# Kernel tuning notes

Measured on AMD Instinct MI355X. Metric: run time of the kernel, lower is better.

Reference implementation:

```python
import jax, jax.numpy as jnp
import numpy as np

B, C, L = 32, 128, 4096
LEVEL = 3
FL = 9            # filter_length (odd so lengths are preserved)
DIM = 512
REG = 0.01        # reg_factor
PAD = (FL - 1) // 2


def _conv1d(x, w, b, padding):
    # x:[B,Cin,L], w:[Cout,Cin,K] -> [B,Cout,L'] (torch cross-correlation)
    y = jax.lax.conv_general_dilated(x, w, (1,), [(padding, padding)],
                                     dimension_numbers=('NCH', 'OIH', 'NCH'))
    return y + b[None, :, None]


def _dywan(approx, stat_w, stat_b, wg1_w, wg1_b, wg2_w, wg2_b):
    feat = jnp.mean(approx, axis=2)                                   # AdaptiveAvgPool1d(1) -> [B,C]
    h = jax.nn.gelu(feat @ stat_w.T + stat_b, approximate=False)
    h = jax.nn.gelu(h @ wg1_w.T + wg1_b, approximate=False)
    filt = h @ wg2_w.T + wg2_b                                        # [B, 2*FL]
    lo_f, hi_f = filt[:, :FL], filt[:, FL:]
    # smoothness: conv1d with kernel [-1,1], zero padding 1 -> forward differences of zero-padded lo_f
    lo_pad = jnp.pad(lo_f, ((0, 0), (1, 1)))
    lo_smooth = jnp.mean(jnp.abs(lo_pad[:, 1:] - lo_pad[:, :-1]))     # length FL+1
    # orthogonality constraint
    lo_n = lo_f / (jnp.linalg.norm(lo_f, axis=1, keepdims=True) + 1e-8)
    shift_loss = 0.0
    for s in (1, 2, 3):
        sh = jnp.roll(lo_n, s, axis=1)
        shift_loss = shift_loss + jnp.mean(jnp.abs(lo_n[:, :, None] * sh[:, None, :]))
    amp_loss = jnp.mean(jnp.abs(jnp.sum(lo_n * lo_n, axis=1) - 1.0))
    ortho = REG * (shift_loss + amp_loss) + 0.1 * lo_smooth
    return lo_f, hi_f, ortho


def _persample_depthwise(x, filt):
    # per-sample filter shared across channels; torch grouped conv groups=B*C.
    # out[b,c,t] = sum_k filt[b,k] * x_pad[b,c,t+k]
    xp = jnp.pad(x, ((0, 0), (0, 0), (PAD, PAD)), mode='edge')        # replicate pad
    Lx = x.shape[2]
    out = jnp.zeros_like(x)
    for k in range(FL):
        out = out + filt[:, k, None, None] * xp[:, :, k:k + Lx]
    return out


def _forward(x, stat_w, stat_b, wg1_w, wg1_b, wg2_w, wg2_b,
             gates_w, gates_b, attn1_w, attn1_b, attn2_w, attn2_b):
    filters = []
    details = []
    approx = x
    ortho_loss = 0.0
    for _ in range(LEVEL):
        lo_f, hi_f, ortho_loss = _dywan(approx, stat_w, stat_b, wg1_w, wg1_b, wg2_w, wg2_b)
        filters.append((lo_f, hi_f))
        new_approx = _persample_depthwise(approx, lo_f)
        detail = _persample_depthwise(approx, hi_f)
        details.append(detail)
        approx = new_approx
    # CrossScaleFusion
    current = approx
    enhanced = []
    for i in range(LEVEL - 1, -1, -1):
        detail = details[i]
        if i < LEVEL - 1:  # attention branches exist only for i < levels-1
            a = jax.nn.gelu(_conv1d(current, attn1_w[i], attn1_b[i], 0), approximate=False)
            attn = jax.nn.sigmoid(_conv1d(a, attn2_w[i], attn2_b[i], 0))
            detail = detail * attn + detail
        gate = jax.nn.sigmoid(_conv1d(current, gates_w[i], gates_b[i], 1))
        current = current + gate * detail
        enhanced.append(detail)
    enhanced.reverse()
    combined = jnp.concatenate([current] + enhanced, axis=1)          # [B,(1+LEVEL)*C,L]
    # ODE is a no-op in the original forward: ode_out = combined
    yl = combined[:, :C, :]
    yh = [combined[:, C * (i + 1):C * (i + 2), :] for i in range(LEVEL)]
    # energy loss under no_grad: dx_dt == 0 -> mse(0, -0) == 0 (computed faithfully)
    cg = jax.lax.stop_gradient(combined)
    dx_dt = jnp.zeros_like(cg)
    dE = 2.0 * jnp.mean(cg * dx_dt, axis=(1, 2))
    diss = jnp.mean(dx_dt * dx_dt, axis=(1, 2))
    energy_loss = jnp.mean((dE + diss) ** 2)
    lo_all = jnp.stack([f[0] for f in filters])                       # [LEVEL,B,FL]
    hi_all = jnp.stack([f[1] for f in filters])
    return yl, yh[0], yh[1], yh[2], ortho_loss, energy_loss, lo_all, hi_all


def setup_inputs() -> dict:
    key = jax.random.key(0)
    ks = jax.random.split(key, 16)
    s = 0.05
    return {
        'x': jax.random.normal(ks[0], (B, C, L), jnp.float32),
        'stat_w': jax.random.normal(ks[1], (DIM, C), jnp.float32) * s,
        'stat_b': jnp.zeros((DIM,), jnp.float32),
        'wg1_w': jax.random.normal(ks[2], (2 * DIM, DIM), jnp.float32) * s,
        'wg1_b': jnp.zeros((2 * DIM,), jnp.float32),
        'wg2_w': jax.random.normal(ks[3], (2 * FL, 2 * DIM), jnp.float32) * s,
        'wg2_b': jnp.zeros((2 * FL,), jnp.float32),
        'gates_w': jax.random.normal(ks[4], (LEVEL, C, C, 3), jnp.float32) * s,
        'gates_b': jnp.zeros((LEVEL, C), jnp.float32),
        'attn1_w': jax.random.normal(ks[5], (LEVEL - 1, C // 4, C, 1), jnp.float32) * s,
        'attn1_b': jnp.zeros((LEVEL - 1, C // 4), jnp.float32),
        'attn2_w': jax.random.normal(ks[6], (LEVEL - 1, C, C // 4, 1), jnp.float32) * s,
        'attn2_b': jnp.zeros((LEVEL - 1, C), jnp.float32),
    }


def reference(x, stat_w, stat_b, wg1_w, wg1_b, wg2_w, wg2_b,
              gates_w, gates_b, attn1_w, attn1_b, attn2_w, attn2_b):
    return _forward(x, stat_w, stat_b, wg1_w, wg1_b, wg2_w, wg2_b,
                    gates_w, gates_b, attn1_w, attn1_b, attn2_w, attn2_b)
```

## Files before the change

kernel.cpp:

```cpp
#include <hip/hip_runtime.h>

#define B_   32
#define C_   128
#define L_   4096
#define FL_  9
#define DIM_ 512
#define BCL  ((size_t)B_ * C_ * L_)

typedef __attribute__((ext_vector_type(8))) short short8;
typedef __attribute__((ext_vector_type(4))) float f32x4;

__device__ __forceinline__ float gelu_f(float x) {
    return 0.5f * x * (1.0f + erff(x * 0.70710678118654752440f));
}
__device__ __forceinline__ float sigm_f(float x) {
    return 1.0f / (1.0f + expf(-x));
}
__device__ __forceinline__ unsigned short bf16_rne(float x) {
    unsigned int u = __float_as_uint(x);
    u += 0x7fffu + ((u >> 16) & 1u);
    return (unsigned short)(u >> 16);
}
__device__ __forceinline__ float bf16_to_f(unsigned short h) {
    return __uint_as_float(((unsigned int)h) << 16);
}

__global__ __launch_bounds__(256) void prep_weights(
    const float* __restrict__ gw, const float* __restrict__ a1w, const float* __restrict__ a2w,
    unsigned short* __restrict__ wgh, unsigned short* __restrict__ wgl,
    unsigned short* __restrict__ a1h, unsigned short* __restrict__ a1l,
    unsigned short* __restrict__ a2h, unsigned short* __restrict__ a2l) {
    int i = blockIdx.x * 256 + threadIdx.x;
    float v; unsigned short* ph; unsigned short* pl; int idx;
    if (i < 147456) {
        int lev = i / 49152, r = i % 49152;
        int co = r / 384, k = r % 384, kp = k >> 7, ci = k & 127;
        v = gw[(((size_t)lev * C_ + co) * C_ + ci) * 3 + kp];
        ph = wgh; pl = wgl; idx = i;
    } else if (i < 147456 + 8192) {
        idx = i - 147456;
        v = a1w[idx];
        ph = a1h; pl = a1l;
    } else if (i < 147456 + 16384) {
        idx = i - 147456 - 8192;
        v = a2w[idx];
        ph = a2h; pl = a2l;
    } else return;
    unsigned short h = bf16_rne(v);
    unsigned short l = bf16_rne(v - bf16_to_f(h));
    ph[idx] = h; pl[idx] = l;
}

__device__ __forceinline__ float block_sum_256(float v, float* red) {
    #pragma unroll
    for (int off = 32; off > 0; off >>= 1) v += __shfl_down(v, off);
    const int wv = threadIdx.x >> 6, ln = threadIdx.x & 63;
    if (ln == 0) red[wv] = v;
    __syncthreads();
    return red[0] + red[1] + red[2] + red[3];
}

__global__ __launch_bounds__(256) void mean_kernel(const float* __restrict__ in,
                                                   float* __restrict__ feat_sum) {
    __shared__ float red[4];
    const int bc = blockIdx.x, t = threadIdx.x;
    const float4* p = (const float4*)(in + (size_t)bc * L_);
    float v = 0.f;
    #pragma unroll
    for (int it = 0; it < L_ / 1024; it++) {
        float4 x = p[t + 256 * it];
        v += x.x + x.y + x.z + x.w;
    }
    float tot = block_sum_256(v, red);
    if (t == 0) feat_sum[bc] = tot;
}

template <int K, int ACT>
__global__ __launch_bounds__(256) void mlp_layer(
    const float* __restrict__ X, const float* __restrict__ W,
    const float* __restrict__ bias, float* __restrict__ Y,
    int N, float xscale) {
    constexpr int PL = K / 64;
    const int w = threadIdx.x >> 6, ln = threadIdx.x & 63;
    const int s = blockIdx.y;
    const int o0 = blockIdx.x * 16 + w * 4;
    float xv[PL];
    const float* xr = X + (size_t)s * K + ln * PL;
    if constexpr (PL == 2) {
        float2 v = *(const float2*)xr;
        xv[0] = v.x * xscale; xv[1] = v.y * xscale;
    } else {
        #pragma unroll
        for (int i = 0; i < PL / 4; i++) {
            float4 v = *(const float4*)(xr + 4 * i);
            xv[4*i] = v.x * xscale; xv[4*i+1] = v.y * xscale;
            xv[4*i+2] = v.z * xscale; xv[4*i+3] = v.w * xscale;
        }
    }
    #pragma unroll
    for (int r = 0; r < 4; r++) {
        int o = o0 + r;
        if (o < N) {
            const float* wr = W + (size_t)o * K + ln * PL;
            float acc = 0.f;
            if constexpr (PL == 2) {
                float2 v = *(const float2*)wr;
                acc = v.x * xv[0] + v.y * xv[1];
            } else {
                #pragma unroll
                for (int i = 0; i < PL / 4; i++) {
                    float4 v = *(const float4*)(wr + 4 * i);
                    acc += v.x * xv[4*i] + v.y * xv[4*i+1] + v.z * xv[4*i+2] + v.w * xv[4*i+3];
                }
            }
            #pragma unroll
            for (int off = 32; off > 0; off >>= 1) acc += __shfl_xor(acc, off);
            if (ln == 0) {
                acc += bias[o];
                Y[(size_t)s * N + o] = ACT ? gelu_f(acc) : acc;
            }
        }
    }
}

__global__ __launch_bounds__(256) void mlp_l3(
    const float* __restrict__ X, const float* __restrict__ W, const float* __restrict__ bias,
    float* __restrict__ lo_out, float* __restrict__ hi_out) {
    constexpr int K = 2 * DIM_, PL = K / 64;
    const int w = threadIdx.x >> 6, ln = threadIdx.x & 63;
    const int s = blockIdx.y;
    const int o0 = blockIdx.x * 16 + w * 4;
    float xv[PL];
    const float* xr = X + (size_t)s * K + ln * PL;
    #pragma unroll
    for (int i = 0; i < PL / 4; i++) {
        float4 v = *(const float4*)(xr + 4 * i);
        xv[4*i] = v.x; xv[4*i+1] = v.y; xv[4*i+2] = v.z; xv[4*i+3] = v.w;
    }
    #pragma unroll
    for (int r = 0; r < 4; r++) {
        int o = o0 + r;
        if (o < 2 * FL_) {
            const float* wr = W + (size_t)o * K + ln * PL;
            float acc = 0.f;
            #pragma unroll
            for (int i = 0; i < PL / 4; i++) {
                float4 v = *(const float4*)(wr + 4 * i);
                acc += v.x * xv[4*i] + v.y * xv[4*i+1] + v.z * xv[4*i+2] + v.w * xv[4*i+3];
            }
            #pragma unroll
            for (int off = 32; off > 0; off >>= 1) acc += __shfl_xor(acc, off);
            if (ln == 0) {
                acc += bias[o];
                if (o < FL_) lo_out[s * FL_ + o] = acc;
                else         hi_out[s * FL_ + (o - FL_)] = acc;
            }
        }
    }
}

__global__ __launch_bounds__(256) void dwconv_kernel(
    const float* __restrict__ in, const float* __restrict__ lo_f, const float* __restrict__ hi_f,
    float* __restrict__ out_lo, float* __restrict__ out_hi, float* __restrict__ feat_next) {
    __shared__ float s[1032];
    __shared__ float red[4];
    const int t = threadIdx.x;
    const int l0 = blockIdx.x * 1024;
    const int c = blockIdx.y, b = blockIdx.z;
    const size_t base = ((size_t)b * C_ + c) * L_;
    *(float4*)&s[4 + 4 * t] = *(const float4*)&in[base + l0 + 4 * t];
    if (t < 4) {
        int gl = l0 - 4 + t;
        s[t] = in[base + max(gl, 0)];
    } else if (t < 8) {
        int i = t - 4;
        s[1028 + i] = in[base + min(l0 + 1024 + i, L_ - 1)];
    }
    float lo[FL_], hi[FL_];
    #pragma unroll
    for (int k = 0; k < FL_; k++) { lo[k] = lo_f[b * FL_ + k]; hi[k] = hi_f[b * FL_ + k]; }
    __syncthreads();
    float oL[4] = {0, 0, 0, 0}, oH[4] = {0, 0, 0, 0};
    #pragma unroll
    for (int k = 0; k < FL_; k++) {
        #pragma unroll
        for (int r = 0; r < 4; r++) {
            float v = s[4 * t + r + k];
            oL[r] += lo[k] * v; oH[r] += hi[k] * v;
        }
    }
    *(float4*)&out_lo[base + l0 + 4 * t] = *(float4*)oL;
    *(float4*)&out_hi[base + l0 + 4 * t] = *(float4*)oH;
    if (feat_next) {
        float tot = block_sum_256(oL[0] + oL[1] + oL[2] + oL[3], red);
        if (t == 0) atomicAdd(&feat_next[b * C_ + c], tot);
    }
}

__global__ void ortho_kernel(const float* __restrict__ lo2, float* __restrict__ scal) {
    const int t = threadIdx.x;
    float smooth = 0.f, sabs2 = 0.f, amp = 0.f;
    if (t < B_) {
        const float* lo = lo2 + t * FL_;
        float ss = 0.f, sa = 0.f, sm = 0.f, prev = 0.f;
        #pragma unroll
        for (int k = 0; k < FL_; k++) {
            float v = lo[k];
            sm += fabsf(v - prev); prev = v;
            ss += v * v; sa += fabsf(v);
        }
        sm += fabsf(prev);
        float den = sqrtf(ss) + 1e-8f;
        float san = sa / den;
        sabs2 = san * san;
        amp = fabsf(ss / (den * den) - 1.0f);
        smooth = sm;
    }
    #pragma unroll
    for (int off = 32; off > 0; off >>= 1) {
        smooth += __shfl_down(smooth, off);
        sabs2  += __shfl_down(sabs2, off);
        amp    += __shfl_down(amp, off);
    }
    if (t == 0) {
        float lo_smooth = smooth / (float)(B_ * 10);
        float shift = 3.0f * (sabs2 / (float)B_) / 81.0f;
        scal[0] = 0.01f * (shift + amp / (float)B_) + 0.1f * lo_smooth;
        scal[1] = 0.0f;
    }
}

#define LT   64
#define SX   136
#define SA   40
template <bool HAS_ATTN>
__global__ __launch_bounds__(256, 2) void recon_kernel(
    const float* __restrict__ cur_in, const float* __restrict__ det_in,
    float* __restrict__ det_out, float* __restrict__ cur_out,
    const unsigned short* __restrict__ wgh, const unsigned short* __restrict__ wgl,
    const float* __restrict__ gb,
    const unsigned short* __restrict__ a1h, const unsigned short* __restrict__ a1l,
    const float* __restrict__ b1,
    const unsigned short* __restrict__ a2h, const unsigned short* __restrict__ a2l,
    const float* __restrict__ b2) {
    __shared__ __attribute__((aligned(16))) unsigned short Xh[(LT + 2) * SX];
    __shared__ __attribute__((aligned(16))) unsigned short Xl[(LT + 2) * SX];
    __shared__ __attribute__((aligned(16))) unsigned short aTh[LT * SA];
    __shared__ __attribute__((aligned(16))) unsigned short aTl[LT * SA];

    const int t = threadIdx.x;
    const int b = blockIdx.y;
    const int l0 = blockIdx.x * LT;
    const float* curb = cur_in + (size_t)b * (C_ * L_);

    for (int u = t; u < 64 * (LT + 2); u += 256) {
        int cp = u / (LT + 2), li = u - cp * (LT + 2);
        int gl = l0 - 1 + li;
        float v0 = 0.f, v1 = 0.f;
        if (gl >= 0 && gl < L_) {
            v0 = curb[(size_t)(2 * cp) * L_ + gl];
            v1 = curb[(size_t)(2 * cp + 1) * L_ + gl];
        }
        unsigned short h0 = bf16_rne(v0), h1 = bf16_rne(v1);
        unsigned short e0 = bf16_rne(v0 - bf16_to_f(h0)), e1 = bf16_rne(v1 - bf16_to_f(h1));
        ((unsigned int*)Xh)[li * (SX / 2) + cp] = (unsigned int)h0 | ((unsigned int)h1 << 16);
        ((unsigned int*)Xl)[li * (SX / 2) + cp] = (unsigned int)e0 | ((unsigned int)e1 << 16);
    }
    __syncthreads();

    const int w = t >> 6, ln = t & 15, q = (t >> 4) & 3;

    f32x4 acc[2][4];
    #pragma unroll
    for (int tm = 0; tm < 2; tm++)
        #pragma unroll
        for (int tn = 0; tn < 4; tn++) acc[tm][tn] = (f32x4){0.f, 0.f, 0.f, 0.f};

    #pragma unroll 2
    for (int kk = 0; kk < 12; kk++) {
        const int kp = kk >> 2, ci0 = (kk & 3) * 32;
        short8 ah[2], al[2];
        #pragma unroll
        for (int tm = 0; tm < 2; tm++) {
            int row = 32 * w + 16 * tm + ln;
            ah[tm] = *(const short8*)&wgh[row * 384 + kk * 32 + q * 8];
            al[tm] = *(const short8*)&wgl[row * 384 + kk * 32 + q * 8];
        }
        #pragma unroll
        for (int tn = 0; tn < 4; tn++) {
            int lrow = 16 * tn + ln + kp;
            const short8 bh = *(const short8*)&Xh[lrow * SX + ci0 + q * 8];
            const short8 bl = *(const short8*)&Xl[lrow * SX + ci0 + q * 8];
            #pragma unroll
            for (int tm = 0; tm < 2; tm++) {
                acc[tm][tn] = __builtin_amdgcn_mfma_f32_16x16x32_bf16(ah[tm], bh, acc[tm][tn], 0, 0, 0);
                acc[tm][tn] = __builtin_amdgcn_mfma_f32_16x16x32_bf16(ah[tm], bl, acc[tm][tn], 0, 0, 0);
                acc[tm][tn] = __builtin_amdgcn_mfma_f32_16x16x32_bf16(al[tm], bh, acc[tm][tn], 0, 0, 0);
            }
        }
    }

    f32x4 dpv[2][4];
    #pragma unroll
    for (int tm = 0; tm < 2; tm++)
        #pragma unroll
        for (int tn = 0; tn < 4; tn++) {
            #pragma unroll
            for (int r = 0; r < 4; r++) {
                int co = 32 * w + 16 * tm + 4 * q + r;
                dpv[tm][tn][r] = det_in[((size_t)b * C_ + co) * L_ + l0 + 16 * tn + ln];
            }
        }

    if (HAS_ATTN) {
        f32x4 acc1[2];
        acc1[0] = (f32x4){0.f, 0.f, 0.f, 0.f};
        acc1[1] = (f32x4){0.f, 0.f, 0.f, 0.f};
        #pragma unroll
        for (int kc = 0; kc < 4; kc++) {
            int ci0 = kc * 32;
            int lrow = 16 * w + ln + 1;
            const short8 bh = *(const short8*)&Xh[lrow * SX + ci0 + q * 8];
            const short8 bl = *(const short8*)&Xl[lrow * SX + ci0 + q * 8];
            #pragma unroll
            for (int tm = 0; tm < 2; tm++) {
                int row = 16 * tm + ln;
                short8 fh = *(const short8*)&a1h[row * 128 + ci0 + q * 8];
                short8 fl = *(const short8*)&a1l[row * 128 + ci0 + q * 8];
                acc1[tm] = __builtin_amdgcn_mfma_f32_16x16x32_bf16(fh, bh, acc1[tm], 0, 0, 0);
                acc1[tm] = __builtin_amdgcn_mfma_f32_16x16x32_bf16(fh, bl, acc1[tm], 0, 0, 0);
                acc1[tm] = __builtin_amdgcn_mfma_f32_16x16x32_bf16(fl, bh, acc1[tm], 0, 0, 0);
            }
        }
        #pragma unroll
        for (int tm = 0; tm < 2; tm++) {
            #pragma unroll
            for (int r = 0; r < 4; r++) {
                int c32 = 16 * tm + 4 * q + r;
                int lcol = 16 * w + ln;
                float v = gelu_f(acc1[tm][r] + b1[c32]);
                unsigned short h = bf16_rne(v);
                aTh[lcol * SA + c32] = h;
                aTl[lcol * SA + c32] = bf16_rne(v - bf16_to_f(h));
            }
        }
        __syncthreads();
        f32x4 acc2[2][4];
        short8 fh2[2], fl2[2];
        #pragma unroll
        for (int tm = 0; tm < 2; tm++) {
            int row = 32 * w + 16 * tm + ln;
            fh2[tm] = *(const short8*)&a2h[row * 32 + q * 8];
            fl2[tm] = *(const short8*)&a2l[row * 32 + q * 8];
            #pragma unroll
            for (int tn = 0; tn < 4; tn++) acc2[tm][tn] = (f32x4){0.f, 0.f, 0.f, 0.f};
        }
        #pragma unroll
        for (int tn = 0; tn < 4; tn++) {
            int lrow = 16 * tn + ln;
            const short8 bh = *(const short8*)&aTh[lrow * SA + q * 8];
            const short8 bl = *(const short8*)&aTl[lrow * SA + q * 8];
            #pragma unroll
            for (int tm = 0; tm < 2; tm++) {
                acc2[tm][tn] = __builtin_amdgcn_mfma_f32_16x16x32_bf16(fh2[tm], bh, acc2[tm][tn], 0, 0, 0);
                acc2[tm][tn] = __builtin_amdgcn_mfma_f32_16x16x32_bf16(fh2[tm], bl, acc2[tm][tn], 0, 0, 0);
                acc2[tm][tn] = __builtin_amdgcn_mfma_f32_16x16x32_bf16(fl2[tm], bh, acc2[tm][tn], 0, 0, 0);
            }
        }
        #pragma unroll
        for (int tm = 0; tm < 2; tm++)
            #pragma unroll
            for (int tn = 0; tn < 4; tn++) {
                #pragma unroll
                for (int r = 0; r < 4; r++) {
                    int co = 32 * w + 16 * tm + 4 * q + r;
                    float at = sigm_f(acc2[tm][tn][r] + b2[co]);
                    float d = dpv[tm][tn][r];
                    d = d * at + d;
                    dpv[tm][tn][r] = d;
                    det_out[((size_t)b * C_ + co) * L_ + l0 + 16 * tn + ln] = d;
                }
            }
    }

    #pragma unroll
    for (int tm = 0; tm < 2; tm++)
        #pragma unroll
        for (int tn = 0; tn < 4; tn++) {
            #pragma unroll
            for (int r = 0; r < 4; r++) {
                int co = 32 * w + 16 * tm + 4 * q + r;
                int lrow = 16 * tn + ln + 1;
                float cur = bf16_to_f(Xh[lrow * SX + co]) + bf16_to_f(Xl[lrow * SX + co]);
                float g = sigm_f(acc[tm][tn][r] + gb[co]);
                cur_out[((size_t)b * C_ + co) * L_ + l0 + 16 * tn + ln] = cur + g * dpv[tm][tn][r];
            }
        }
}

static inline void run_mlp(const float* feat, const float* stat_w, const float* stat_b,
                           const float* wg1_w, const float* wg1_b,
                           const float* wg2_w, const float* wg2_b,
                           float* h1_g, float* h2_g, float* lo_out, float* hi_out,
                           hipStream_t stream) {
    mlp_layer<C_, 1><<<dim3(DIM_ / 16, B_), 256, 0, stream>>>(
        feat, stat_w, stat_b, h1_g, DIM_, 1.0f / (float)L_);
    mlp_layer<DIM_, 1><<<dim3(2 * DIM_ / 16, B_), 256, 0, stream>>>(
        h1_g, wg1_w, wg1_b, h2_g, 2 * DIM_, 1.0f);
    mlp_l3<<<dim3(2, B_), 256, 0, stream>>>(h2_g, wg2_w, wg2_b, lo_out, hi_out);
}

extern "C" void kernel_launch(void* const* d_in, const int* in_sizes, int n_in,
                              void* d_out, int out_size, void* d_ws, size_t ws_size,
                              hipStream_t stream) {
    (void)in_sizes; (void)n_in; (void)out_size; (void)ws_size;
    const float* x       = (const float*)d_in[0];
    const float* stat_w  = (const float*)d_in[1];
    const float* stat_b  = (const float*)d_in[2];
    const float* wg1_w   = (const float*)d_in[3];
    const float* wg1_b   = (const float*)d_in[4];
    const float* wg2_w   = (const float*)d_in[5];
    const float* wg2_b   = (const float*)d_in[6];
    const float* gates_w = (const float*)d_in[7];
    const float* gates_b = (const float*)d_in[8];
    const float* a1w     = (const float*)d_in[9];
    const float* a1b     = (const float*)d_in[10];
    const float* a2w     = (const float*)d_in[11];
    const float* a2b     = (const float*)d_in[12];

    float* out = (float*)d_out;
    float* yl  = out;
    float* yh0 = out + BCL;
    float* yh1 = out + 2 * BCL;
    float* yh2 = out + 3 * BCL;
    float* scal = out + 4 * BCL;
    float* lo_all = scal + 2;
    float* hi_all = lo_all + 3 * B_ * FL_;

    float* wsA   = (float*)d_ws;
    float* featA = wsA + BCL;
    float* featB = featA + B_ * C_;
    float* h1_g  = featB + B_ * C_;
    float* h2_g  = h1_g + B_ * DIM_;
    unsigned short* wgh = (unsigned short*)(h2_g + B_ * 2 * DIM_);
    unsigned short* wgl = wgh + 147456;
    unsigned short* a1h = wgl + 147456;
    unsigned short* a1l = a1h + 8192;
    unsigned short* a2h = a1l + 8192;
    unsigned short* a2l = a2h + 8192;

    prep_weights<<<dim3((147456 + 16384 + 255) / 256), 256, 0, stream>>>(
        gates_w, a1w, a2w, wgh, wgl, a1h, a1l, a2h, a2l);

    const dim3 cgrid(L_ / 1024, C_, B_);
    const dim3 rgrid(L_ / LT, B_);

    mean_kernel<<<dim3(B_ * C_), 256, 0, stream>>>(x, featA);
    run_mlp(featA, stat_w, stat_b, wg1_w, wg1_b, wg2_w, wg2_b, h1_g, h2_g,
            lo_all, hi_all, stream);
    hipMemsetAsync(featB, 0, B_ * C_ * sizeof(float), stream);
    dwconv_kernel<<<cgrid, 256, 0, stream>>>(x, lo_all, hi_all, wsA, yh0, featB);
    run_mlp(featB, stat_w, stat_b, wg1_w, wg1_b, wg2_w, wg2_b, h1_g, h2_g,
            lo_all + B_ * FL_, hi_all + B_ * FL_, stream);
    hipMemsetAsync(featA, 0, B_ * C_ * sizeof(float), stream);
    dwconv_kernel<<<cgrid, 256, 0, stream>>>(wsA, lo_all + B_ * FL_, hi_all + B_ * FL_, yl, yh1, featA);
    run_mlp(featA, stat_w, stat_b, wg1_w, wg1_b, wg2_w, wg2_b, h1_g, h2_g,
            lo_all + 2 * B_ * FL_, hi_all + 2 * B_ * FL_, stream);
    dwconv_kernel<<<cgrid, 256, 0, stream>>>(yl, lo_all + 2 * B_ * FL_, hi_all + 2 * B_ * FL_,
                                             wsA, yh2, nullptr);
    ortho_kernel<<<dim3(1), 64, 0, stream>>>(lo_all + 2 * B_ * FL_, scal);
    recon_kernel<false><<<rgrid, 256, 0, stream>>>(wsA, yh2, nullptr, yl,
        wgh + 2 * 49152, wgl + 2 * 49152, gates_b + 2 * C_,
        nullptr, nullptr, nullptr, nullptr, nullptr, nullptr);
    recon_kernel<true><<<rgrid, 256, 0, stream>>>(yl, yh1, yh1, wsA,
        wgh + 1 * 49152, wgl + 1 * 49152, gates_b + 1 * C_,
        a1h + 4096, a1l + 4096, a1b + 32,
        a2h + 4096, a2l + 4096, a2b + C_);
    recon_kernel<true><<<rgrid, 256, 0, stream>>>(wsA, yh0, yh0, yl,
        wgh, wgl, gates_b,
        a1h, a1l, a1b,
        a2h, a2l, a2b);
}
```

Baseline: 768.5 us.

## Fuse three reconstruction levels into one kernel with halo recompute

```diff
diff --git a/kernel.cpp b/kernel.cpp
--- a/kernel.cpp
+++ b/kernel.cpp
@@ -161,7 +161,8 @@
 
 __global__ __launch_bounds__(256) void dwconv_kernel(
     const float* __restrict__ in, const float* __restrict__ lo_f, const float* __restrict__ hi_f,
-    float* __restrict__ out_lo, float* __restrict__ out_hi, float* __restrict__ feat_next) {
+    float* __restrict__ out_lo, float* __restrict__ out_hi, float* __restrict__ feat_next,
+    float* __restrict__ Hout) {
     __shared__ float s[1032];
     __shared__ float red[4];
     const int t = threadIdx.x;
@@ -191,6 +192,12 @@
     }
     *(float4*)&out_lo[base + l0 + 4 * t] = *(float4*)oL;
     *(float4*)&out_hi[base + l0 + 4 * t] = *(float4*)oH;
+    if (Hout) {
+        int p0 = l0 + 4 * t;
+        if ((p0 & 63) == 0)  Hout[(((size_t)b * C_ + c) * 64 + (p0 >> 6)) * 2 + 0] = oH[0];
+        int p3 = p0 + 3;
+        if ((p3 & 63) == 63) Hout[(((size_t)b * C_ + c) * 64 + (p3 >> 6)) * 2 + 1] = oH[3];
+    }
     if (feat_next) {
         float tot = block_sum_256(oL[0] + oL[1] + oL[2] + oL[3], red);
         if (t == 0) atomicAdd(&feat_next[b * C_ + c], tot);
@@ -231,31 +238,32 @@
 }
 
 #define LT   64
+#define XR   82
+#define NT   5
 #define SX   136
 #define SA   40
-template <bool HAS_ATTN>
-__global__ __launch_bounds__(256, 2) void recon_kernel(
-    const float* __restrict__ cur_in, const float* __restrict__ det_in,
-    float* __restrict__ det_out, float* __restrict__ cur_out,
+__global__ __launch_bounds__(256, 2) void recon_fused(
+    const float* __restrict__ cur_in, const float* __restrict__ det2,
+    float* det1, const float* __restrict__ det1H, float* det0,
+    float* __restrict__ cur_out,
     const unsigned short* __restrict__ wgh, const unsigned short* __restrict__ wgl,
     const float* __restrict__ gb,
     const unsigned short* __restrict__ a1h, const unsigned short* __restrict__ a1l,
     const float* __restrict__ b1,
     const unsigned short* __restrict__ a2h, const unsigned short* __restrict__ a2l,
     const float* __restrict__ b2) {
-    __shared__ __attribute__((aligned(16))) unsigned short Xh[(LT + 2) * SX];
-    __shared__ __attribute__((aligned(16))) unsigned short Xl[(LT + 2) * SX];
-    __shared__ __attribute__((aligned(16))) unsigned short aTh[LT * SA];
-    __shared__ __attribute__((aligned(16))) unsigned short aTl[LT * SA];
-
-    const int t = threadIdx.x;
-    const int b = blockIdx.y;
-    const int l0 = blockIdx.x * LT;
+    __shared__ __attribute__((aligned(16))) unsigned short Xh[XR * SX];
+    __shared__ __attribute__((aligned(16))) unsigned short Xl[XR * SX];
+    __shared__ __attribute__((aligned(16))) unsigned short aTh[80 * SA];
+    __shared__ __attribute__((aligned(16))) unsigned short aTl[80 * SA];
+
+    const int t = threadIdx.x, b = blockIdx.y, T = blockIdx.x;
+    const int l0 = T * LT;
     const float* curb = cur_in + (size_t)b * (C_ * L_);
 
-    for (int u = t; u < 64 * (LT + 2); u += 256) {
-        int cp = u / (LT + 2), li = u - cp * (LT + 2);
-        int gl = l0 - 1 + li;
+    for (int u = t; u < 64 * XR; u += 256) {
+        int cp = u / XR, li = u - cp * XR;
+        int gl = l0 - 5 + li;
         float v0 = 0.f, v1 = 0.f;
         if (gl >= 0 && gl < L_) {
             v0 = curb[(size_t)(2 * cp) * L_ + gl];
@@ -270,132 +278,213 @@
 
     const int w = t >> 6, ln = t & 15, q = (t >> 4) & 3;
 
-    f32x4 acc[2][4];
+    float cur[2][NT][4];
     #pragma unroll
     for (int tm = 0; tm < 2; tm++)
         #pragma unroll
-        for (int tn = 0; tn < 4; tn++) acc[tm][tn] = (f32x4){0.f, 0.f, 0.f, 0.f};
-
-    #pragma unroll 2
-    for (int kk = 0; kk < 12; kk++) {
-        const int kp = kk >> 2, ci0 = (kk & 3) * 32;
-        short8 ah[2], al[2];
-        #pragma unroll
-        for (int tm = 0; tm < 2; tm++) {
-            int row = 32 * w + 16 * tm + ln;
-            ah[tm] = *(const short8*)&wgh[row * 384 + kk * 32 + q * 8];
-            al[tm] = *(const short8*)&wgl[row * 384 + kk * 32 + q * 8];
-        }
-        #pragma unroll
-        for (int tn = 0; tn < 4; tn++) {
-            int lrow = 16 * tn + ln + kp;
-            const short8 bh = *(const short8*)&Xh[lrow * SX + ci0 + q * 8];
-            const short8 bl = *(const short8*)&Xl[lrow * SX + ci0 + q * 8];
-            #pragma unroll
-            for (int tm = 0; tm < 2; tm++) {
-                acc[tm][tn] = __builtin_amdgcn_mfma_f32_16x16x32_bf16(ah[tm], bh, acc[tm][tn], 0, 0, 0);
-                acc[tm][tn] = __builtin_amdgcn_mfma_f32_16x16x32_bf16(ah[tm], bl, acc[tm][tn], 0, 0, 0);
-                acc[tm][tn] = __builtin_amdgcn_mfma_f32_16x16x32_bf16(al[tm], bh, acc[tm][tn], 0, 0, 0);
-            }
-        }
-    }
-
-    f32x4 dpv[2][4];
-    #pragma unroll
-    for (int tm = 0; tm < 2; tm++)
-        #pragma unroll
-        for (int tn = 0; tn < 4; tn++) {
-            #pragma unroll
-            for (int r = 0; r < 4; r++) {
-                int co = 32 * w + 16 * tm + 4 * q + r;
-                dpv[tm][tn][r] = det_in[((size_t)b * C_ + co) * L_ + l0 + 16 * tn + ln];
-            }
-        }
-
-    if (HAS_ATTN) {
-        f32x4 acc1[2];
-        acc1[0] = (f32x4){0.f, 0.f, 0.f, 0.f};
-        acc1[1] = (f32x4){0.f, 0.f, 0.f, 0.f};
-        #pragma unroll
-        for (int kc = 0; kc < 4; kc++) {
-            int ci0 = kc * 32;
-            int lrow = 16 * w + ln + 1;
-            const short8 bh = *(const short8*)&Xh[lrow * SX + ci0 + q * 8];
-            const short8 bl = *(const short8*)&Xl[lrow * SX + ci0 + q * 8];
-            #pragma unroll
-            for (int tm = 0; tm < 2; tm++) {
-                int row = 16 * tm + ln;
-                short8 fh = *(const short8*)&a1h[row * 128 + ci0 + q * 8];
-                short8 fl = *(const short8*)&a1l[row * 128 + ci0 + q * 8];
-                acc1[tm] = __builtin_amdgcn_mfma_f32_16x16x32_bf16(fh, bh, acc1[tm], 0, 0, 0);
-                acc1[tm] = __builtin_amdgcn_mfma_f32_16x16x32_bf16(fh, bl, acc1[tm], 0, 0, 0);
-                acc1[tm] = __builtin_amdgcn_mfma_f32_16x16x32_bf16(fl, bh, acc1[tm], 0, 0, 0);
-            }
-        }
-        #pragma unroll
-        for (int tm = 0; tm < 2; tm++) {
-            #pragma unroll
-            for (int r = 0; r < 4; r++) {
-                int c32 = 16 * tm + 4 * q + r;
-                int lcol = 16 * w + ln;
-                float v = gelu_f(acc1[tm][r] + b1[c32]);
-                unsigned short h = bf16_rne(v);
-                aTh[lcol * SA + c32] = h;
-                aTl[lcol * SA + c32] = bf16_rne(v - bf16_to_f(h));
-            }
-        }
-        __syncthreads();
-        f32x4 acc2[2][4];
-        short8 fh2[2], fl2[2];
-        #pragma unroll
-        for (int tm = 0; tm < 2; tm++) {
-            int row = 32 * w + 16 * tm + ln;
-            fh2[tm] = *(const short8*)&a2h[row * 32 + q * 8];
-            fl2[tm] = *(const short8*)&a2l[row * 32 + q * 8];
-            #pragma unroll
-            for (int tn = 0; tn < 4; tn++) acc2[tm][tn] = (f32x4){0.f, 0.f, 0.f, 0.f};
-        }
-        #pragma unroll
-        for (int tn = 0; tn < 4; tn++) {
-            int lrow = 16 * tn + ln;
-            const short8 bh = *(const short8*)&aTh[lrow * SA + q * 8];
-            const short8 bl = *(const short8*)&aTl[lrow * SA + q * 8];
-            #pragma unroll
-            for (int tm = 0; tm < 2; tm++) {
-                acc2[tm][tn] = __builtin_amdgcn_mfma_f32_16x16x32_bf16(fh2[tm], bh, acc2[tm][tn], 0, 0, 0);
-                acc2[tm][tn] = __builtin_amdgcn_mfma_f32_16x16x32_bf16(fh2[tm], bl, acc2[tm][tn], 0, 0, 0);
-                acc2[tm][tn] = __builtin_amdgcn_mfma_f32_16x16x32_bf16(fl2[tm], bh, acc2[tm][tn], 0, 0, 0);
-            }
-        }
+        for (int tn = 0; tn < NT; tn++) {
+            int cp0 = 16 * w + 8 * tm + 2 * q;
+            int lp = 16 * tn + ln + 1;
+            #pragma unroll
+            for (int pr = 0; pr < 2; pr++) {
+                unsigned int uh = ((unsigned int*)Xh)[lp * (SX / 2) + cp0 + pr];
+                unsigned int ul = ((unsigned int*)Xl)[lp * (SX / 2) + cp0 + pr];
+                cur[tm][tn][2 * pr]     = bf16_to_f((unsigned short)(uh & 0xffff)) +
+                                          bf16_to_f((unsigned short)(ul & 0xffff));
+                cur[tm][tn][2 * pr + 1] = bf16_to_f((unsigned short)(uh >> 16)) +
+                                          bf16_to_f((unsigned short)(ul >> 16));
+            }
+        }
+
+    for (int s = 0; s < 3; s++) {
+        const int lev = 2 - s;
+        const unsigned short* wh = wgh + lev * 49152;
+        const unsigned short* wl = wgl + lev * 49152;
+        const float* gbb = gb + lev * C_;
+
+        float dv[2][NT][4];
         #pragma unroll
         for (int tm = 0; tm < 2; tm++)
             #pragma unroll
-            for (int tn = 0; tn < 4; tn++) {
+            for (int tn = 0; tn < NT; tn++)
                 #pragma unroll
                 for (int r = 0; r < 4; r++) {
                     int co = 32 * w + 16 * tm + 4 * q + r;
-                    float at = sigm_f(acc2[tm][tn][r] + b2[co]);
-                    float d = dpv[tm][tn][r];
-                    d = d * at + d;
-                    dpv[tm][tn][r] = d;
-                    det_out[((size_t)b * C_ + co) * L_ + l0 + 16 * tn + ln] = d;
-                }
-            }
-    }
-
-    #pragma unroll
-    for (int tm = 0; tm < 2; tm++)
-        #pragma unroll
-        for (int tn = 0; tn < 4; tn++) {
-            #pragma unroll
-            for (int r = 0; r < 4; r++) {
-                int co = 32 * w + 16 * tm + 4 * q + r;
-                int lrow = 16 * tn + ln + 1;
-                float cur = bf16_to_f(Xh[lrow * SX + co]) + bf16_to_f(Xl[lrow * SX + co]);
-                float g = sigm_f(acc[tm][tn][r] + gb[co]);
-                cur_out[((size_t)b * C_ + co) * L_ + l0 + 16 * tn + ln] = cur + g * dpv[tm][tn][r];
-            }
-        }
+                    int off = 16 * tn + ln;
+                    int gl = l0 + off - 4;
+                    float d = 0.f;
+                    if (s == 0) {
+                        if (gl >= 0 && gl < L_) d = det2[((size_t)b * C_ + co) * L_ + gl];
+                    } else if (s == 1) {
+                        if (off >= 4 && off < 68) d = det1[((size_t)b * C_ + co) * L_ + gl];
+                        else if (off == 3 && T > 0)   d = det1H[(((size_t)b * C_ + co) * 64 + (T - 1)) * 2 + 1];
+                        else if (off == 68 && T < 63) d = det1H[(((size_t)b * C_ + co) * 64 + (T + 1)) * 2 + 0];
+                    } else {
+                        if (off >= 4 && off < 68) d = det0[((size_t)b * C_ + co) * L_ + gl];
+                    }
+                    dv[tm][tn][r] = d;
+                }
+
+        f32x4 acc[2][NT];
+        #pragma unroll
+        for (int tm = 0; tm < 2; tm++)
+            #pragma unroll
+            for (int tn = 0; tn < NT; tn++) acc[tm][tn] = (f32x4){0.f, 0.f, 0.f, 0.f};
+
+        #pragma unroll 2
+        for (int kk = 0; kk < 12; kk++) {
+            const int kp = kk >> 2, ci0 = (kk & 3) * 32;
+            short8 ah[2], al[2];
+            #pragma unroll
+            for (int tm = 0; tm < 2; tm++) {
+                int row = 32 * w + 16 * tm + ln;
+                ah[tm] = *(const short8*)&wh[row * 384 + kk * 32 + q * 8];
+                al[tm] = *(const short8*)&wl[row * 384 + kk * 32 + q * 8];
+            }
+            #pragma unroll
+            for (int tn = 0; tn < NT; tn++) {
+                int lrow = 16 * tn + ln + kp;
+                const short8 bh = *(const short8*)&Xh[lrow * SX + ci0 + q * 8];
+                const short8 bl = *(const short8*)&Xl[lrow * SX + ci0 + q * 8];
+                #pragma unroll
+                for (int tm = 0; tm < 2; tm++) {
+                    acc[tm][tn] = __builtin_amdgcn_mfma_f32_16x16x32_bf16(ah[tm], bh, acc[tm][tn], 0, 0, 0);
+                    acc[tm][tn] = __builtin_amdgcn_mfma_f32_16x16x32_bf16(ah[tm], bl, acc[tm][tn], 0, 0, 0);
+                    acc[tm][tn] = __builtin_amdgcn_mfma_f32_16x16x32_bf16(al[tm], bh, acc[tm][tn], 0, 0, 0);
+                }
+            }
+        }
+
+        if (s >= 1) {
+            const int ao = (s == 1) ? 4096 : 0;
+            const unsigned short* A1h = a1h + ao; const unsigned short* A1l = a1l + ao;
+            const float* B1 = b1 + ((s == 1) ? 32 : 0);
+            const unsigned short* A2h = a2h + ao; const unsigned short* A2l = a2l + ao;
+            const float* B2 = b2 + ((s == 1) ? C_ : 0);
+
+            for (int u2 = w; u2 < 2 * NT; u2 += 4) {
+                int tile = u2 >> 1, ch = u2 & 1;
+                f32x4 a1c = (f32x4){0.f, 0.f, 0.f, 0.f};
+                #pragma unroll
+                for (int kc = 0; kc < 4; kc++) {
+                    int ci0 = kc * 32;
+                    int lrow = 16 * tile + ln + 1;
+                    const short8 bh = *(const short8*)&Xh[lrow * SX + ci0 + q * 8];
+                    const short8 bl = *(const short8*)&Xl[lrow * SX + ci0 + q * 8];
+                    int row = 16 * ch + ln;
+                    short8 fh = *(const short8*)&A1h[row * 128 + ci0 + q * 8];
+                    short8 fl = *(const short8*)&A1l[row * 128 + ci0 + q * 8];
+                    a1c = __builtin_amdgcn_mfma_f32_16x16x32_bf16(fh, bh, a1c, 0, 0, 0);
+                    a1c = __builtin_amdgcn_mfma_f32_16x16x32_bf16(fh, bl, a1c, 0, 0, 0);
+                    a1c = __builtin_amdgcn_mfma_f32_16x16x32_bf16(fl, bh, a1c, 0, 0, 0);
+                }
+                #pragma unroll
+                for (int r = 0; r < 4; r++) {
+                    int c32 = 16 * ch + 4 * q + r;
+                    int lcol = 16 * tile + ln;
+                    float v = gelu_f(a1c[r] + B1[c32]);
+                    unsigned short h = bf16_rne(v);
+                    aTh[lcol * SA + c32] = h;
+                    aTl[lcol * SA + c32] = bf16_rne(v - bf16_to_f(h));
+                }
+            }
+            __syncthreads();
+
+            short8 fh2[2], fl2[2];
+            #pragma unroll
+            for (int tm = 0; tm < 2; tm++) {
+                int row = 32 * w + 16 * tm + ln;
+                fh2[tm] = *(const short8*)&A2h[row * 32 + q * 8];
+                fl2[tm] = *(const short8*)&A2l[row * 32 + q * 8];
+            }
+            #pragma unroll
+            for (int tn = 0; tn < NT; tn++) {
+                int lrow = 16 * tn + ln;
+                const short8 bh = *(const short8*)&aTh[lrow * SA + q * 8];
+                const short8 bl = *(const short8*)&aTl[lrow * SA + q * 8];
+                f32x4 c2[2];
+                c2[0] = (f32x4){0.f, 0.f, 0.f, 0.f};
+                c2[1] = (f32x4){0.f, 0.f, 0.f, 0.f};
+                #pragma unroll
+                for (int tm = 0; tm < 2; tm++) {
+                    c2[tm] = __builtin_amdgcn_mfma_f32_16x16x32_bf16(fh2[tm], bh, c2[tm], 0, 0, 0);
+                    c2[tm] = __builtin_amdgcn_mfma_f32_16x16x32_bf16(fh2[tm], bl, c2[tm], 0, 0, 0);
+                    c2[tm] = __builtin_amdgcn_mfma_f32_16x16x32_bf16(fl2[tm], bh, c2[tm], 0, 0, 0);
+                }
+                #pragma unroll
+                for (int tm = 0; tm < 2; tm++)
+                    #pragma unroll
+                    for (int r = 0; r < 4; r++) {
+                        int co = 32 * w + 16 * tm + 4 * q + r;
+                        float at = sigm_f(c2[tm][r] + B2[co]);
+                        dv[tm][tn][r] = dv[tm][tn][r] * (1.f + at);
+                    }
+            }
+
+            float* dd = (s == 1) ? det1 : det0;
+            #pragma unroll
+            for (int tm = 0; tm < 2; tm++)
+                #pragma unroll
+                for (int tn = 0; tn < NT; tn++) {
+                    int off = 16 * tn + ln;
+                    if (off >= 4 && off < 68) {
+                        int gl = l0 + off - 4;
+                        #pragma unroll
+                        for (int r = 0; r < 4; r++) {
+                            int co = 32 * w + 16 * tm + 4 * q + r;
+                            dd[((size_t)b * C_ + co) * L_ + gl] = dv[tm][tn][r];
+                        }
+                    }
+                }
+        }
+
+        #pragma unroll
+        for (int tm = 0; tm < 2; tm++)
+            #pragma unroll
+            for (int tn = 0; tn < NT; tn++)
+                #pragma unroll
+                for (int r = 0; r < 4; r++) {
+                    int co = 32 * w + 16 * tm + 4 * q + r;
+                    float g = sigm_f(acc[tm][tn][r] + gbb[co]);
+                    cur[tm][tn][r] += g * dv[tm][tn][r];
+                }
+
+        if (s < 2) {
+            __syncthreads();
+            #pragma unroll
+            for (int tm = 0; tm < 2; tm++)
+                #pragma unroll
+                for (int tn = 0; tn < NT; tn++) {
+                    int lp = 16 * tn + ln + 1;
+                    int cp0 = 16 * w + 8 * tm + 2 * q;
+                    #pragma unroll
+                    for (int pr = 0; pr < 2; pr++) {
+                        float v0 = cur[tm][tn][2 * pr], v1 = cur[tm][tn][2 * pr + 1];
+                        unsigned short h0 = bf16_rne(v0), h1 = bf16_rne(v1);
+                        unsigned short e0 = bf16_rne(v0 - bf16_to_f(h0));
+                        unsigned short e1 = bf16_rne(v1 - bf16_to_f(h1));
+                        ((unsigned int*)Xh)[lp * (SX / 2) + cp0 + pr] = (unsigned int)h0 | ((unsigned int)h1 << 16);
+                        ((unsigned int*)Xl)[lp * (SX / 2) + cp0 + pr] = (unsigned int)e0 | ((unsigned int)e1 << 16);
+                    }
+                }
+            __syncthreads();
+        } else {
+            #pragma unroll
+            for (int tm = 0; tm < 2; tm++)
+                #pragma unroll
+                for (int tn = 0; tn < NT; tn++) {
+                    int off = 16 * tn + ln;
+                    if (off >= 4 && off < 68) {
+                        int gl = l0 + off - 4;
+                        #pragma unroll
+                        for (int r = 0; r < 4; r++) {
+                            int co = 32 * w + 16 * tm + 4 * q + r;
+                            cur_out[((size_t)b * C_ + co) * L_ + gl] = cur[tm][tn][r];
+                        }
+                    }
+                }
+        }
+    }
 }
 
 static inline void run_mlp(const float* feat, const float* stat_w, const float* stat_b,
@@ -448,35 +537,30 @@
     unsigned short* a1l = a1h + 8192;
     unsigned short* a2h = a1l + 8192;
     unsigned short* a2l = a2h + 8192;
+    float* det1H = (float*)(a2l + 8192);
 
     prep_weights<<<dim3((147456 + 16384 + 255) / 256), 256, 0, stream>>>(
         gates_w, a1w, a2w, wgh, wgl, a1h, a1l, a2h, a2l);
 
     const dim3 cgrid(L_ / 1024, C_, B_);
-    const dim3 rgrid(L_ / LT, B_);
 
     mean_kernel<<<dim3(B_ * C_), 256, 0, stream>>>(x, featA);
     run_mlp(featA, stat_w, stat_b, wg1_w, wg1_b, wg2_w, wg2_b, h1_g, h2_g,
             lo_all, hi_all, stream);
     hipMemsetAsync(featB, 0, B_ * C_ * sizeof(float), stream);
-    dwconv_kernel<<<cgrid, 256, 0, stream>>>(x, lo_all, hi_all, wsA, yh0, featB);
+    dwconv_kernel<<<cgrid, 256, 0, stream>>>(x, lo_all, hi_all, wsA, yh0, featB, nullptr);
     run_mlp(featB, stat_w, stat_b, wg1_w, wg1_b, wg2_w, wg2_b, h1_g, h2_g,
             lo_all + B_ * FL_, hi_all + B_ * FL_, stream);
     hipMemsetAsync(featA, 0, B_ * C_ * sizeof(float), stream);
-    dwconv_kernel<<<cgrid, 256, 0, stream>>>(wsA, lo_all + B_ * FL_, hi_all + B_ * FL_, yl, yh1, featA);
+    dwconv_kernel<<<cgrid, 256, 0, stream>>>(wsA, lo_all + B_ * FL_, hi_all + B_ * FL_,
+                                             yl, yh1, featA, det1H);
     run_mlp(featA, stat_w, stat_b, wg1_w, wg1_b, wg2_w, wg2_b, h1_g, h2_g,
             lo_all + 2 * B_ * FL_, hi_all + 2 * B_ * FL_, stream);
     dwconv_kernel<<<cgrid, 256, 0, stream>>>(yl, lo_all + 2 * B_ * FL_, hi_all + 2 * B_ * FL_,
-                                             wsA, yh2, nullptr);
+                                             wsA, yh2, nullptr, nullptr);
     ortho_kernel<<<dim3(1), 64, 0, stream>>>(lo_all + 2 * B_ * FL_, scal);
-    recon_kernel<false><<<rgrid, 256, 0, stream>>>(wsA, yh2, nullptr, yl,
-        wgh + 2 * 49152, wgl + 2 * 49152, gates_b + 2 * C_,
-        nullptr, nullptr, nullptr, nullptr, nullptr, nullptr);
-    recon_kernel<true><<<rgrid, 256, 0, stream>>>(yl, yh1, yh1, wsA,
-        wgh + 1 * 49152, wgl + 1 * 49152, gates_b + 1 * C_,
-        a1h + 4096, a1l + 4096, a1b + 32,
-        a2h + 4096, a2l + 4096, a2b + C_);
-    recon_kernel<true><<<rgrid, 256, 0, stream>>>(wsA, yh0, yh0, yl,
+    recon_fused<<<dim3(L_ / LT, B_), 256, 0, stream>>>(
+        wsA, yh2, yh1, det1H, yh0, yl,
         wgh, wgl, gates_b,
         a1h, a1l, a1b,
         a2h, a2l, a2b);
```

Result: slower. 1.162 ms (+51.3%).
